# Kernel tuning notes

Measured on AMD Instinct MI355X. Metric: run time of the kernel, lower is better.

The kernel has to match this reference:

```python
import jax, jax.numpy as jnp
import numpy as np

B, S, D, H = 4, 2048, 1024, 16
DK = D // H


def setup_inputs() -> dict:
    key = jax.random.key(0)
    ks = jax.random.split(key, 7)
    s = 1.0 / np.sqrt(D)
    return {
        "q": jax.random.normal(ks[0], (B, S, D), jnp.float32),
        "k": jax.random.normal(ks[1], (B, S, D), jnp.float32),
        "v": jax.random.normal(ks[2], (B, S, D), jnp.float32),
        "Wq": jax.random.normal(ks[3], (D, D), jnp.float32) * s,
        "Wk": jax.random.normal(ks[4], (D, D), jnp.float32) * s,
        "Wv": jax.random.normal(ks[5], (D, D), jnp.float32) * s,
        "Wo": jax.random.normal(ks[6], (D, D), jnp.float32) * s,
    }


def _split(x):
    # [B,S,D] -> [B,H,S,DK]
    return x.reshape(B, S, H, DK).transpose(0, 2, 1, 3)


def reference(q, k, v, Wq, Wk, Wv, Wo):
    # Linear projections (nn.Linear with bias=False: x @ W^T)
    qh = _split(q @ Wq.T)
    kh = _split(k @ Wk.T)
    vh = _split(v @ Wv.T)
    scale = 1.0 / jnp.sqrt(jnp.asarray(DK, qh.dtype))
    # attention scores [B,H,S,S]
    attn = jnp.einsum("bhqd,bhkd->bhqk", qh, kh) * scale
    # causal mask: disallow k > q
    causal = jnp.tril(jnp.ones((S, S), dtype=bool))
    attn = jnp.where(causal[None, None], attn, -jnp.inf)
    attn = jax.nn.softmax(attn, axis=-1)  # dropout p=0.0 -> identity
    out = jnp.einsum("bhqk,bhkd->bhqd", attn, vh)
    # combine heads [B,H,S,DK] -> [B,S,D]
    out = out.transpose(0, 2, 1, 3).reshape(B, S, D)
    return out @ Wo.T
```

## Files before the change

### kernel.cpp

```cpp
#include <hip/hip_runtime.h>
#include <math.h>
#include <stdint.h>

#define B_  4
#define S_  2048
#define D_  1024
#define H_  16
#define DK_ 64
#define NR_ (B_ * S_)

typedef _Float16 half8  __attribute__((ext_vector_type(8)));
typedef _Float16 half4  __attribute__((ext_vector_type(4)));
typedef float    floatx4 __attribute__((ext_vector_type(4)));

__global__ __launch_bounds__(256)
void split_w4(const float* __restrict__ w0, const float* __restrict__ w1,
              const float* __restrict__ w2, const float* __restrict__ w3,
              _Float16* __restrict__ wbase, int n8) {
    const int i = blockIdx.x * 256 + threadIdx.x;
    if (i >= n8) return;
    const float* src = (blockIdx.y == 0) ? w0 : (blockIdx.y == 1) ? w1 :
                       (blockIdx.y == 2) ? w2 : w3;
    _Float16* hi = wbase + (size_t)blockIdx.y * 2 * ((size_t)D_ * D_);
    _Float16* lo = hi + (size_t)D_ * D_;
    const float4* s4 = (const float4*)src;
    float4 a = s4[2 * i];
    float4 b = s4[2 * i + 1];
    float f[8] = {a.x, a.y, a.z, a.w, b.x, b.y, b.z, b.w};
    union { half8 v; _Float16 h[8]; } H, L;
    #pragma unroll
    for (int j = 0; j < 8; ++j) {
        _Float16 h = (_Float16)f[j];
        H.h[j] = h;
        L.h[j] = (_Float16)(f[j] - (float)h);
    }
    *(half8*)(hi + (size_t)i * 8) = H.v;
    *(half8*)(lo + (size_t)i * 8) = L.v;
}

#define GBN 128
#define GBM 128
#define GBK 32
#define LDH 40

template <int APACK>
__global__ __launch_bounds__(256, 3)
void gemm_xwt_mfma(const void* __restrict__ Xin,
                   const _Float16* __restrict__ Wh, const _Float16* __restrict__ Wl,
                   void* __restrict__ out0, int mode) {
    __shared__ __align__(16) _Float16 Whi[GBM][LDH];
    __shared__ __align__(16) _Float16 Wlo[GBM][LDH];
    const int K = D_;

    const int tid  = threadIdx.x;
    const int wave = tid >> 6;
    const int lane = tid & 63;
    const int row16 = lane & 15;
    const int quad  = lane >> 4;
    const int n0 = blockIdx.x * GBN;
    const int m0 = blockIdx.y * GBM;

    const int wrow = tid >> 1;
    const int wc   = (tid & 1) << 4;

    const float*    aFb = (const float*)Xin +
                          (size_t)(n0 + wave * 32 + row16) * K + quad * 8;
    const uint32_t* aPb = (const uint32_t*)Xin +
                          (size_t)(n0 + wave * 32 + row16) * K + quad * 8;

    floatx4 acc[2][8];
    const floatx4 zero4 = {0.f, 0.f, 0.f, 0.f};
    #pragma unroll
    for (int i = 0; i < 2; ++i)
        #pragma unroll
        for (int j = 0; j < 8; ++j) acc[i][j] = zero4;

    half8 pa_h[2], pa_l[2];
    uint4 wh0, wh1, wl0, wl1;
    auto load_regs = [&](int k0) {
        #pragma unroll
        for (int ni = 0; ni < 2; ++ni) {
            if (APACK == 0) {
                const float* p = aFb + (size_t)ni * 16 * K + k0;
                float4 f0 = *(const float4*)p;
                float4 f1 = *(const float4*)(p + 4);
                float f[8] = {f0.x, f0.y, f0.z, f0.w, f1.x, f1.y, f1.z, f1.w};
                union { half8 v; _Float16 h[8]; } hi, lo;
                #pragma unroll
                for (int j = 0; j < 8; ++j) {
                    _Float16 h = (_Float16)f[j];
                    hi.h[j] = h;
                    lo.h[j] = (_Float16)(f[j] - (float)h);
                }
                pa_h[ni] = hi.v;
                pa_l[ni] = lo.v;
            } else {
                const uint32_t* p = aPb + (size_t)ni * 16 * K + k0;
                uint32_t u[8];
                *(uint4*)&u[0] = *(const uint4*)p;
                *(uint4*)&u[4] = *(const uint4*)(p + 4);
                union { half8 v; uint16_t s[8]; } hi, lo;
                #pragma unroll
                for (int j = 0; j < 8; ++j) {
                    hi.s[j] = (uint16_t)(u[j] & 0xffffu);
                    lo.s[j] = (uint16_t)(u[j] >> 16);
                }
                pa_h[ni] = hi.v;
                pa_l[ni] = lo.v;
            }
        }
        const _Float16* pwh = Wh + (size_t)(m0 + wrow) * K + k0 + wc;
        const _Float16* pwl = Wl + (size_t)(m0 + wrow) * K + k0 + wc;
        wh0 = *(const uint4*)pwh;
        wh1 = *(const uint4*)(pwh + 8);
        wl0 = *(const uint4*)pwl;
        wl1 = *(const uint4*)(pwl + 8);
    };

    load_regs(0);
    for (int k0 = 0; k0 < K; k0 += GBK) {
        half8 a_hi[2] = {pa_h[0], pa_h[1]};
        half8 a_lo[2] = {pa_l[0], pa_l[1]};
        __syncthreads();
        *(uint4*)&Whi[wrow][wc]     = wh0;
        *(uint4*)&Whi[wrow][wc + 8] = wh1;
        *(uint4*)&Wlo[wrow][wc]     = wl0;
        *(uint4*)&Wlo[wrow][wc + 8] = wl1;
        __syncthreads();
        if (k0 + GBK < K) load_regs(k0 + GBK);

        #pragma unroll
        for (int mj = 0; mj < 8; ++mj) {
            const int r = mj * 16 + row16;
            half8 b_hi = *(const half8*)&Whi[r][quad * 8];
            half8 b_lo = *(const half8*)&Wlo[r][quad * 8];
            #pragma unroll
            for (int ni = 0; ni < 2; ++ni) {
                acc[ni][mj] = __builtin_amdgcn_mfma_f32_16x16x32_f16(
                    a_hi[ni], b_hi, acc[ni][mj], 0, 0, 0);
                acc[ni][mj] = __builtin_amdgcn_mfma_f32_16x16x32_f16(
                    a_hi[ni], b_lo, acc[ni][mj], 0, 0, 0);
                acc[ni][mj] = __builtin_amdgcn_mfma_f32_16x16x32_f16(
                    a_lo[ni], b_hi, acc[ni][mj], 0, 0, 0);
            }
        }
    }

    #pragma unroll
    for (int ni = 0; ni < 2; ++ni)
        #pragma unroll
        for (int mj = 0; mj < 8; ++mj) {
            if (mode == 2) {
                const int s  = n0 + wave * 32 + ni * 16 + quad * 4;
                const int b  = s >> 11;
                const int sr = s & (S_ - 1);
                const int m  = m0 + mj * 16 + row16;
                const int h  = m >> 6;
                const int dk = m & 63;
                half4 h4;
                #pragma unroll
                for (int r = 0; r < 4; ++r) h4[r] = (_Float16)acc[ni][mj][r];
                *(half4*)((_Float16*)out0 +
                          (((size_t)b * H_ + h) * DK_ + dk) * S_ + sr) = h4;
            } else {
                #pragma unroll
                for (int rg = 0; rg < 4; ++rg) {
                    const int n = n0 + wave * 32 + ni * 16 + quad * 4 + rg;
                    const int m = m0 + mj * 16 + row16;
                    const float v = acc[ni][mj][rg];
                    if (mode == 0) {
                        ((float*)out0)[(size_t)n * D_ + m] = v;
                    } else {
                        const int b  = n >> 11;
                        const int s  = n & (S_ - 1);
                        const int h  = m >> 6;
                        const int dk = m & 63;
                        union { _Float16 h16; uint16_t u; } hi, lo;
                        hi.h16 = (_Float16)v;
                        lo.h16 = (_Float16)(v - (float)hi.h16);
                        uint32_t u = ((uint32_t)lo.u << 16) | (uint32_t)hi.u;
                        ((uint32_t*)out0)[(((size_t)b * H_ + h) * S_ + s) * DK_ + dk] = u;
                    }
                }
            }
        }
}

__global__ __launch_bounds__(256)
void attn_mfma(const uint32_t* __restrict__ Qhl, const uint32_t* __restrict__ Khl,
               const _Float16* __restrict__ Vth, uint32_t* __restrict__ Ahl) {
    __shared__ __align__(16) _Float16 KhiC[64][64];
    __shared__ __align__(16) _Float16 KloC[64][64];
    __shared__ __align__(16) _Float16 VC[64][64];
    __shared__ __align__(16) _Float16 PCT[4][16][72];

    const int bh = blockIdx.y;
    const int qt = (int)(gridDim.x - 1) - (int)blockIdx.x;
    const int q0 = qt * 64;
    const int tid  = threadIdx.x;
    const int wave = tid >> 6;
    const int lane = tid & 63;
    const int c    = lane & 15;
    const int quad = lane >> 4;

    const uint32_t* Kb = Khl + (size_t)bh * S_ * DK_;
    const _Float16* Vb = Vth + (size_t)bh * DK_ * S_;

    half8 qhi[2], qlo[2];
    {
        const uint32_t* Qrow = Qhl + ((size_t)bh * S_ + q0 + wave * 16 + c) * DK_;
        #pragma unroll
        for (int ks = 0; ks < 2; ++ks) {
            uint32_t u[8];
            *(uint4*)&u[0] = *(const uint4*)(Qrow + ks * 32 + quad * 8);
            *(uint4*)&u[4] = *(const uint4*)(Qrow + ks * 32 + quad * 8 + 4);
            union { half8 v; uint16_t s[8]; } hi, lo;
            #pragma unroll
            for (int j = 0; j < 8; ++j) {
                hi.s[j] = (uint16_t)(u[j] & 0xffffu);
                lo.s[j] = (uint16_t)(u[j] >> 16);
            }
            qhi[ks] = hi.v; qlo[ks] = lo.v;
        }
    }

    floatx4 acc_o[4];
    const floatx4 zero4 = {0.f, 0.f, 0.f, 0.f};
    #pragma unroll
    for (int dt = 0; dt < 4; ++dt) acc_o[dt] = zero4;
    float mrun = -INFINITY, lrun = 0.f;

    const int srow = tid >> 2;
    const int soff = (tid & 3) * 16;
    const int ch0  = (tid & 3) * 2;

    uint4 ku[4];
    uint4 vv[2];
    auto load_tile = [&](int kt) {
        const uint4* ksrc = (const uint4*)(Kb + (size_t)(kt * 64 + srow) * DK_ + soff);
        ku[0] = ksrc[0]; ku[1] = ksrc[1]; ku[2] = ksrc[2]; ku[3] = ksrc[3];
        const uint4* vsrc = (const uint4*)(Vb + (size_t)srow * S_ + kt * 64 + soff);
        vv[0] = vsrc[0]; vv[1] = vsrc[1];
    };
    auto write_tile = [&]() {
        #pragma unroll
        for (int hf = 0; hf < 2; ++hf) {
            const int swz = ((ch0 + hf) ^ (srow & 7)) * 8;
            uint32_t uu[8];
            *(uint4*)&uu[0] = ku[2 * hf];
            *(uint4*)&uu[4] = ku[2 * hf + 1];
            union { half8 v; uint16_t s[8]; } hi, lo;
            #pragma unroll
            for (int j = 0; j < 8; ++j) {
                hi.s[j] = (uint16_t)(uu[j] & 0xffffu);
                lo.s[j] = (uint16_t)(uu[j] >> 16);
            }
            *(half8*)&KhiC[srow][swz] = hi.v;
            *(half8*)&KloC[srow][swz] = lo.v;
            *(uint4*)&VC[srow][swz]   = vv[hf];
        }
    };

    const int qmy = q0 + wave * 16 + c;
    const floatx4 neg4 = {-INFINITY, -INFINITY, -INFINITY, -INFINITY};

    load_tile(0);
    write_tile();

    for (int kt = 0; kt <= qt; ++kt) {
        const int k0 = kt * 64;
        const bool diag = (kt == qt);
        __syncthreads();
        if (kt < qt) load_tile(kt + 1);

        floatx4 sc[4];
        #pragma unroll
        for (int t = 0; t < 4; ++t) {
            if (diag && t > wave) { sc[t] = neg4; continue; }
            floatx4 s4 = zero4;
            const int krow = t * 16 + c;
            #pragma unroll
            for (int ks = 0; ks < 2; ++ks) {
                const int swz = ((ks * 4 + quad) ^ (krow & 7)) * 8;
                half8 kb = *(const half8*)&KhiC[krow][swz];
                half8 kl = *(const half8*)&KloC[krow][swz];
                s4 = __builtin_amdgcn_mfma_f32_16x16x32_f16(kb, qhi[ks], s4, 0, 0, 0);
                s4 = __builtin_amdgcn_mfma_f32_16x16x32_f16(kl, qhi[ks], s4, 0, 0, 0);
                s4 = __builtin_amdgcn_mfma_f32_16x16x32_f16(kb, qlo[ks], s4, 0, 0, 0);
            }
            #pragma unroll
            for (int r = 0; r < 4; ++r) s4[r] *= 0.125f;
            if (diag && t == wave) {
                #pragma unroll
                for (int r = 0; r < 4; ++r) {
                    const int k = k0 + t * 16 + quad * 4 + r;
                    if (k > qmy) s4[r] = -INFINITY;
                }
            }
            sc[t] = s4;
        }

        float mx = -INFINITY;
        #pragma unroll
        for (int t = 0; t < 4; ++t)
            #pragma unroll
            for (int r = 0; r < 4; ++r) mx = fmaxf(mx, sc[t][r]);
        mx = fmaxf(mx, __shfl_xor(mx, 16));
        mx = fmaxf(mx, __shfl_xor(mx, 32));
        const float mnew  = fmaxf(mrun, mx);
        const float alpha = __expf(mrun - mnew);
        float ls = 0.f;
        #pragma unroll
        for (int t = 0; t < 4; ++t) {
            half4 p4;
            #pragma unroll
            for (int r = 0; r < 4; ++r) {
                const float p = __expf(sc[t][r] - mnew);
                ls += p;
                p4[r] = (_Float16)p;
            }
            *(half4*)&PCT[wave][c][t * 16 + quad * 4] = p4;
        }
        lrun = alpha * lrun + ls;
        mrun = mnew;
        #pragma unroll
        for (int dt = 0; dt < 4; ++dt)
            #pragma unroll
            for (int r = 0; r < 4; ++r) acc_o[dt][r] *= alpha;

        #pragma unroll
        for (int kc = 0; kc < 2; ++kc) {
            if (diag && kc == 1 && wave < 2) continue;
            half8 pb = *(const half8*)&PCT[wave][c][kc * 32 + quad * 8];
            #pragma unroll
            for (int dt = 0; dt < 4; ++dt) {
                const int vrow = dt * 16 + c;
                const int swz = ((kc * 4 + quad) ^ (vrow & 7)) * 8;
                half8 va = *(const half8*)&VC[vrow][swz];
                acc_o[dt] = __builtin_amdgcn_mfma_f32_16x16x32_f16(va, pb, acc_o[dt], 0, 0, 0);
            }
        }

        __syncthreads();
        if (kt < qt) write_tile();
    }

    float l = lrun;
    l += __shfl_xor(l, 16);
    l += __shfl_xor(l, 32);
    const float inv = 1.f / l;
    const int b = bh >> 4, h = bh & 15;
    uint32_t* dstA = Ahl + ((size_t)b * S_ + qmy) * D_ + h * DK_;
    #pragma unroll
    for (int dt = 0; dt < 4; ++dt) {
        uint4 pk;
        #pragma unroll
        for (int r = 0; r < 4; ++r) {
            const float o = acc_o[dt][r] * inv;
            union { _Float16 h16; uint16_t u; } hi, lo;
            hi.h16 = (_Float16)o;
            lo.h16 = (_Float16)(o - (float)hi.h16);
            ((uint32_t*)&pk)[r] = ((uint32_t)lo.u << 16) | (uint32_t)hi.u;
        }
        *(uint4*)(dstA + dt * 16 + quad * 4) = pk;
    }
}

extern "C" void kernel_launch(void* const* d_in, const int* in_sizes, int n_in,
                              void* d_out, int out_size, void* d_ws, size_t ws_size,
                              hipStream_t stream) {
    const float* q  = (const float*)d_in[0];
    const float* k  = (const float*)d_in[1];
    const float* v  = (const float*)d_in[2];
    const float* Wq = (const float*)d_in[3];
    const float* Wk = (const float*)d_in[4];
    const float* Wv = (const float*)d_in[5];
    const float* Wo = (const float*)d_in[6];
    float* out = (float*)d_out;

    const size_t SZ  = (size_t)B_ * S_ * D_;
    const size_t WSZ = (size_t)D_ * D_;

    _Float16* ws    = (_Float16*)d_ws;
    _Float16* wbase = ws;
    uint32_t* Qhl = (uint32_t*)(wbase + 8 * WSZ);
    uint32_t* Khl = (uint32_t*)(wbase + 8 * WSZ + 2 * SZ);
    _Float16* Vth = wbase + 8 * WSZ + 4 * SZ;
    uint32_t* Ahl = (uint32_t*)(wbase + 8 * WSZ + 5 * SZ);

    _Float16* wq_hi = wbase + 0 * 2 * WSZ, *wq_lo = wq_hi + WSZ;
    _Float16* wk_hi = wbase + 1 * 2 * WSZ, *wk_lo = wk_hi + WSZ;
    _Float16* wv_hi = wbase + 2 * 2 * WSZ, *wv_lo = wv_hi + WSZ;
    _Float16* wo_hi = wbase + 3 * 2 * WSZ, *wo_lo = wo_hi + WSZ;

    const int nw8 = (int)(WSZ / 8);
    dim3 gb(NR_ / GBN, D_ / GBM);
    dim3 ga(S_ / 64, B_ * H_);
    dim3 gw(nw8 / 256, 4);

    split_w4<<<gw, 256, 0, stream>>>(Wq, Wk, Wv, Wo, wbase, nw8);

    gemm_xwt_mfma<0><<<gb, 256, 0, stream>>>(q, wq_hi, wq_lo, Qhl, 1);
    gemm_xwt_mfma<0><<<gb, 256, 0, stream>>>(k, wk_hi, wk_lo, Khl, 1);
    gemm_xwt_mfma<0><<<gb, 256, 0, stream>>>(v, wv_hi, wv_lo, Vth, 2);

    attn_mfma<<<ga, 256, 0, stream>>>(Qhl, Khl, Vth, Ahl);

    gemm_xwt_mfma<1><<<gb, 256, 0, stream>>>(Ahl, wo_hi, wo_lo, out, 0);
}
```

Measured before the change: 578.7 us.

## Process two 64-row query tiles per attention block to reuse K/V tiles

Each attention workgroup now handles 128 query rows as two 64-row sub-tiles sharing every K/V tile staged into shared memory, and the grid along the query dimension is halved. This halves K/V global loads and LDS staging per query row and amortizes the per-tile barriers. In exchange each thread keeps twice the Q fragments, accumulators and softmax state, which raises register pressure and may lower occupancy. The grid also becomes coarser (1024 blocks), with less even causal load balance.

After: 593.3 us. +2.5%, slower.

```diff
diff --git a/kernel.cpp b/kernel.cpp
--- a/kernel.cpp
+++ b/kernel.cpp
@@ -195,8 +195,8 @@
     __shared__ __align__(16) _Float16 PCT[4][16][72];
 
     const int bh = blockIdx.y;
-    const int qt = (int)(gridDim.x - 1) - (int)blockIdx.x;
-    const int q0 = qt * 64;
+    const int g  = (int)(gridDim.x - 1) - (int)blockIdx.x;
+    const int q0 = g * 128;
     const int tid  = threadIdx.x;
     const int wave = tid >> 6;
     const int lane = tid & 63;
@@ -206,29 +206,34 @@
     const uint32_t* Kb = Khl + (size_t)bh * S_ * DK_;
     const _Float16* Vb = Vth + (size_t)bh * DK_ * S_;
 
-    half8 qhi[2], qlo[2];
-    {
-        const uint32_t* Qrow = Qhl + ((size_t)bh * S_ + q0 + wave * 16 + c) * DK_;
+    half8 qhi[2][2], qlo[2][2];
+    #pragma unroll
+    for (int s = 0; s < 2; ++s) {
+        const uint32_t* Qrow = Qhl +
+            ((size_t)bh * S_ + q0 + s * 64 + wave * 16 + c) * DK_;
         #pragma unroll
         for (int ks = 0; ks < 2; ++ks) {
             uint32_t u[8];
             *(uint4*)&u[0] = *(const uint4*)(Qrow + ks * 32 + quad * 8);
             *(uint4*)&u[4] = *(const uint4*)(Qrow + ks * 32 + quad * 8 + 4);
-            union { half8 v; uint16_t s[8]; } hi, lo;
+            union { half8 v; uint16_t s16[8]; } hi, lo;
             #pragma unroll
             for (int j = 0; j < 8; ++j) {
-                hi.s[j] = (uint16_t)(u[j] & 0xffffu);
-                lo.s[j] = (uint16_t)(u[j] >> 16);
-            }
-            qhi[ks] = hi.v; qlo[ks] = lo.v;
+                hi.s16[j] = (uint16_t)(u[j] & 0xffffu);
+                lo.s16[j] = (uint16_t)(u[j] >> 16);
+            }
+            qhi[s][ks] = hi.v; qlo[s][ks] = lo.v;
         }
     }
 
-    floatx4 acc_o[4];
+    floatx4 acc_o[2][4];
     const floatx4 zero4 = {0.f, 0.f, 0.f, 0.f};
     #pragma unroll
-    for (int dt = 0; dt < 4; ++dt) acc_o[dt] = zero4;
-    float mrun = -INFINITY, lrun = 0.f;
+    for (int s = 0; s < 2; ++s)
+        #pragma unroll
+        for (int dt = 0; dt < 4; ++dt) acc_o[s][dt] = zero4;
+    float mrun[2] = {-INFINITY, -INFINITY};
+    float lrun[2] = {0.f, 0.f};
 
     const int srow = tid >> 2;
     const int soff = (tid & 3) * 16;
@@ -249,11 +254,11 @@
             uint32_t uu[8];
             *(uint4*)&uu[0] = ku[2 * hf];
             *(uint4*)&uu[4] = ku[2 * hf + 1];
-            union { half8 v; uint16_t s[8]; } hi, lo;
+            union { half8 v; uint16_t s16[8]; } hi, lo;
             #pragma unroll
             for (int j = 0; j < 8; ++j) {
-                hi.s[j] = (uint16_t)(uu[j] & 0xffffu);
-                lo.s[j] = (uint16_t)(uu[j] >> 16);
+                hi.s16[j] = (uint16_t)(uu[j] & 0xffffu);
+                lo.s16[j] = (uint16_t)(uu[j] >> 16);
             }
             *(half8*)&KhiC[srow][swz] = hi.v;
             *(half8*)&KloC[srow][swz] = lo.v;
@@ -261,108 +266,119 @@
         }
     };
 
-    const int qmy = q0 + wave * 16 + c;
     const floatx4 neg4 = {-INFINITY, -INFINITY, -INFINITY, -INFINITY};
+    const int KT = 2 * g + 2;
 
     load_tile(0);
     write_tile();
 
-    for (int kt = 0; kt <= qt; ++kt) {
+    for (int kt = 0; kt < KT; ++kt) {
         const int k0 = kt * 64;
-        const bool diag = (kt == qt);
         __syncthreads();
-        if (kt < qt) load_tile(kt + 1);
-
-        floatx4 sc[4];
-        #pragma unroll
-        for (int t = 0; t < 4; ++t) {
-            if (diag && t > wave) { sc[t] = neg4; continue; }
-            floatx4 s4 = zero4;
-            const int krow = t * 16 + c;
-            #pragma unroll
-            for (int ks = 0; ks < 2; ++ks) {
-                const int swz = ((ks * 4 + quad) ^ (krow & 7)) * 8;
-                half8 kb = *(const half8*)&KhiC[krow][swz];
-                half8 kl = *(const half8*)&KloC[krow][swz];
-                s4 = __builtin_amdgcn_mfma_f32_16x16x32_f16(kb, qhi[ks], s4, 0, 0, 0);
-                s4 = __builtin_amdgcn_mfma_f32_16x16x32_f16(kl, qhi[ks], s4, 0, 0, 0);
-                s4 = __builtin_amdgcn_mfma_f32_16x16x32_f16(kb, qlo[ks], s4, 0, 0, 0);
-            }
-            #pragma unroll
-            for (int r = 0; r < 4; ++r) s4[r] *= 0.125f;
-            if (diag && t == wave) {
+        if (kt + 1 < KT) load_tile(kt + 1);
+
+        #pragma unroll
+        for (int s = 0; s < 2; ++s) {
+            if (s == 0 && kt == KT - 1) continue;
+            const bool diag = (kt == 2 * g + s);
+            const int qmy = q0 + s * 64 + wave * 16 + c;
+
+            floatx4 sc[4];
+            #pragma unroll
+            for (int t = 0; t < 4; ++t) {
+                if (diag && t > wave) { sc[t] = neg4; continue; }
+                floatx4 s4 = zero4;
+                const int krow = t * 16 + c;
+                #pragma unroll
+                for (int ks = 0; ks < 2; ++ks) {
+                    const int swz = ((ks * 4 + quad) ^ (krow & 7)) * 8;
+                    half8 kb = *(const half8*)&KhiC[krow][swz];
+                    half8 kl = *(const half8*)&KloC[krow][swz];
+                    s4 = __builtin_amdgcn_mfma_f32_16x16x32_f16(kb, qhi[s][ks], s4, 0, 0, 0);
+                    s4 = __builtin_amdgcn_mfma_f32_16x16x32_f16(kl, qhi[s][ks], s4, 0, 0, 0);
+                    s4 = __builtin_amdgcn_mfma_f32_16x16x32_f16(kb, qlo[s][ks], s4, 0, 0, 0);
+                }
+                #pragma unroll
+                for (int r = 0; r < 4; ++r) s4[r] *= 0.125f;
+                if (diag && t == wave) {
+                    #pragma unroll
+                    for (int r = 0; r < 4; ++r) {
+                        const int k = k0 + t * 16 + quad * 4 + r;
+                        if (k > qmy) s4[r] = -INFINITY;
+                    }
+                }
+                sc[t] = s4;
+            }
+
+            float mx = -INFINITY;
+            #pragma unroll
+            for (int t = 0; t < 4; ++t)
+                #pragma unroll
+                for (int r = 0; r < 4; ++r) mx = fmaxf(mx, sc[t][r]);
+            mx = fmaxf(mx, __shfl_xor(mx, 16));
+            mx = fmaxf(mx, __shfl_xor(mx, 32));
+            const float mnew  = fmaxf(mrun[s], mx);
+            const float alpha = __expf(mrun[s] - mnew);
+            float ls = 0.f;
+            #pragma unroll
+            for (int t = 0; t < 4; ++t) {
+                half4 p4;
                 #pragma unroll
                 for (int r = 0; r < 4; ++r) {
-                    const int k = k0 + t * 16 + quad * 4 + r;
-                    if (k > qmy) s4[r] = -INFINITY;
-                }
-            }
-            sc[t] = s4;
-        }
-
-        float mx = -INFINITY;
-        #pragma unroll
-        for (int t = 0; t < 4; ++t)
-            #pragma unroll
-            for (int r = 0; r < 4; ++r) mx = fmaxf(mx, sc[t][r]);
-        mx = fmaxf(mx, __shfl_xor(mx, 16));
-        mx = fmaxf(mx, __shfl_xor(mx, 32));
-        const float mnew  = fmaxf(mrun, mx);
-        const float alpha = __expf(mrun - mnew);
-        float ls = 0.f;
-        #pragma unroll
-        for (int t = 0; t < 4; ++t) {
-            half4 p4;
+                    const float p = __expf(sc[t][r] - mnew);
+                    ls += p;
+                    p4[r] = (_Float16)p;
+                }
+                *(half4*)&PCT[wave][c][t * 16 + quad * 4] = p4;
+            }
+            lrun[s] = alpha * lrun[s] + ls;
+            mrun[s] = mnew;
+            #pragma unroll
+            for (int dt = 0; dt < 4; ++dt)
+                #pragma unroll
+                for (int r = 0; r < 4; ++r) acc_o[s][dt][r] *= alpha;
+
+            #pragma unroll
+            for (int kc = 0; kc < 2; ++kc) {
+                if (diag && kc == 1 && wave < 2) continue;
+                half8 pb = *(const half8*)&PCT[wave][c][kc * 32 + quad * 8];
+                #pragma unroll
+                for (int dt = 0; dt < 4; ++dt) {
+                    const int vrow = dt * 16 + c;
+                    const int swz = ((kc * 4 + quad) ^ (vrow & 7)) * 8;
+                    half8 va = *(const half8*)&VC[vrow][swz];
+                    acc_o[s][dt] = __builtin_amdgcn_mfma_f32_16x16x32_f16(
+                        va, pb, acc_o[s][dt], 0, 0, 0);
+                }
+            }
+        }
+
+        __syncthreads();
+        if (kt + 1 < KT) write_tile();
+    }
+
+    const int b = bh >> 4, h = bh & 15;
+    #pragma unroll
+    for (int s = 0; s < 2; ++s) {
+        float l = lrun[s];
+        l += __shfl_xor(l, 16);
+        l += __shfl_xor(l, 32);
+        const float inv = 1.f / l;
+        const int qmy = q0 + s * 64 + wave * 16 + c;
+        uint32_t* dstA = Ahl + ((size_t)b * S_ + qmy) * D_ + h * DK_;
+        #pragma unroll
+        for (int dt = 0; dt < 4; ++dt) {
+            uint4 pk;
             #pragma unroll
             for (int r = 0; r < 4; ++r) {
-                const float p = __expf(sc[t][r] - mnew);
-                ls += p;
-                p4[r] = (_Float16)p;
-            }
-            *(half4*)&PCT[wave][c][t * 16 + quad * 4] = p4;
-        }
-        lrun = alpha * lrun + ls;
-        mrun = mnew;
-        #pragma unroll
-        for (int dt = 0; dt < 4; ++dt)
-            #pragma unroll
-            for (int r = 0; r < 4; ++r) acc_o[dt][r] *= alpha;
-
-        #pragma unroll
-        for (int kc = 0; kc < 2; ++kc) {
-            if (diag && kc == 1 && wave < 2) continue;
-            half8 pb = *(const half8*)&PCT[wave][c][kc * 32 + quad * 8];
-            #pragma unroll
-            for (int dt = 0; dt < 4; ++dt) {
-                const int vrow = dt * 16 + c;
-                const int swz = ((kc * 4 + quad) ^ (vrow & 7)) * 8;
-                half8 va = *(const half8*)&VC[vrow][swz];
-                acc_o[dt] = __builtin_amdgcn_mfma_f32_16x16x32_f16(va, pb, acc_o[dt], 0, 0, 0);
-            }
-        }
-
-        __syncthreads();
-        if (kt < qt) write_tile();
-    }
-
-    float l = lrun;
-    l += __shfl_xor(l, 16);
-    l += __shfl_xor(l, 32);
-    const float inv = 1.f / l;
-    const int b = bh >> 4, h = bh & 15;
-    uint32_t* dstA = Ahl + ((size_t)b * S_ + qmy) * D_ + h * DK_;
-    #pragma unroll
-    for (int dt = 0; dt < 4; ++dt) {
-        uint4 pk;
-        #pragma unroll
-        for (int r = 0; r < 4; ++r) {
-            const float o = acc_o[dt][r] * inv;
-            union { _Float16 h16; uint16_t u; } hi, lo;
-            hi.h16 = (_Float16)o;
-            lo.h16 = (_Float16)(o - (float)hi.h16);
-            ((uint32_t*)&pk)[r] = ((uint32_t)lo.u << 16) | (uint32_t)hi.u;
-        }
-        *(uint4*)(dstA + dt * 16 + quad * 4) = pk;
+                const float o = acc_o[s][dt][r] * inv;
+                union { _Float16 h16; uint16_t u; } hi, lo;
+                hi.h16 = (_Float16)o;
+                lo.h16 = (_Float16)(o - (float)hi.h16);
+                ((uint32_t*)&pk)[r] = ((uint32_t)lo.u << 16) | (uint32_t)hi.u;
+            }
+            *(uint4*)(dstA + dt * 16 + quad * 4) = pk;
+        }
     }
 }
 
@@ -395,7 +411,7 @@
 
     const int nw8 = (int)(WSZ / 8);
     dim3 gb(NR_ / GBN, D_ / GBM);
-    dim3 ga(S_ / 64, B_ * H_);
+    dim3 ga(S_ / 128, B_ * H_);
     dim3 gw(nw8 / 256, 4);
 
     split_w4<<<gw, 256, 0, stream>>>(Wq, Wk, Wv, Wo, wbase, nw8);
```
